# Kernel tuning notes

Hardware: AMD Instinct MI355X
Metric: run time of the kernel (lower is better)

The kernel has to match this reference:

```python
import jax, jax.numpy as jnp
import numpy as np

B, T, D, H = 2048, 1024, 64, 32  # batch, timesteps, input_size, hidden_dim


def setup_inputs() -> dict:
    key = jax.random.key(0)
    ks = jax.random.split(key, 11)
    k = 1.0 / np.sqrt(H)  # torch default GRU/Linear init range
    u = lambda kk, shape: jax.random.uniform(kk, shape, jnp.float32, -k, k)
    return {
        "x": jax.random.normal(ks[0], (B, T, D), jnp.float32),
        # layer 0 (input D -> hidden H); gate order r,z,n as in torch
        "w_ih0": u(ks[1], (3 * H, D)), "w_hh0": u(ks[2], (3 * H, H)),
        "b_ih0": u(ks[3], (3 * H,)),   "b_hh0": u(ks[4], (3 * H,)),
        # layer 1 (hidden H -> hidden H)
        "w_ih1": u(ks[5], (3 * H, H)), "w_hh1": u(ks[6], (3 * H, H)),
        "b_ih1": u(ks[7], (3 * H,)),   "b_hh1": u(ks[8], (3 * H,)),
        # classifier head H -> 1
        "w_cls": u(ks[9], (1, H)), "b_cls": u(ks[10], (1,)),
    }


def _gru_layer(x, w_ih, w_hh, b_ih, b_hh):
    # x: [B, T, Din]. Precompute the input contribution for all steps in one GEMM.
    gx = jnp.einsum('btd,gd->btg', x, w_ih) + b_ih  # [B, T, 3H]
    h0 = jnp.zeros((x.shape[0], H), x.dtype)

    def step(h, gx_t):
        gh = h @ w_hh.T + b_hh                       # [B, 3H]
        xr, xz, xn = jnp.split(gx_t, 3, axis=-1)
        hr, hz, hn = jnp.split(gh, 3, axis=-1)
        r = jax.nn.sigmoid(xr + hr)
        z = jax.nn.sigmoid(xz + hz)
        n = jnp.tanh(xn + r * hn)
        h_new = (1.0 - z) * n + z * h                # torch GRU update
        return h_new, h_new

    h_last, hs = jax.lax.scan(step, h0, jnp.swapaxes(gx, 0, 1))  # scan over T
    return jnp.swapaxes(hs, 0, 1), h_last            # [B, T, H], [B, H]


def reference(x, w_ih0, w_hh0, b_ih0, b_hh0, w_ih1, w_hh1, b_ih1, b_hh1, w_cls, b_cls):
    out0, h_last0 = _gru_layer(x, w_ih0, w_hh0, b_ih0, b_hh0)
    out1, h_last1 = _gru_layer(out0, w_ih1, w_hh1, b_ih1, b_hh1)
    y = jax.nn.sigmoid(h_last1 @ w_cls.T + b_cls)    # [B, 1]
    hidden = jnp.stack([h_last0, h_last1], axis=0)   # [2, B, H], like torch GRU hidden
    return y, hidden
```

## Files before the change

kernel.cpp:

```cpp
#include <hip/hip_runtime.h>
#include <hip/hip_bf16.h>

#define B_ 2048
#define T_ 1024

typedef short short8 __attribute__((ext_vector_type(8)));
typedef float floatx4 __attribute__((ext_vector_type(4)));

#define MFMA16(a, b, c) __builtin_amdgcn_mfma_f32_16x16x32_bf16((a), (b), (c), 0, 0, 0)
#define NLOG2E -1.4426950408889634f
#define TWOLOG2E 2.8853900817779268f

__device__ __forceinline__ unsigned short f2bf(float f) {
  union { float f; unsigned int i; } v;
  v.f = f;
  unsigned int r = v.i + 0x7fffu + ((v.i >> 16) & 1u);
  return (unsigned short)(r >> 16);
}

__device__ __forceinline__ unsigned int pack2(float lo, float hi) {
  __hip_bfloat162 h2;
  h2.x = __float2bfloat16(lo);
  h2.y = __float2bfloat16(hi);
  union { __hip_bfloat162 h; unsigned int u; } v;
  v.h = h2;
  return v.u;
}

__device__ __forceinline__ int rho32(int pb) {
  return 8 * ((pb >> 2) & 3) + 4 * (pb >> 4) + (pb & 3);
}

__device__ __forceinline__ short8 load_wfrag(const float* W, int K,
                                             int mt, int kt, int q, int c) {
  int p = 16 * mt + c;
  int blk = p >> 5;
  int pb = p & 31;
  int tr = 32 * blk + rho32(pb);
  float s = (blk < 2) ? NLOG2E : TWOLOG2E;
  const float* src = W + tr * K + 32 * kt + 8 * q;
  short8 out;
#pragma unroll
  for (int j = 0; j < 8; j++) out[j] = (short)f2bf(src[j] * s);
  return out;
}

__device__ __forceinline__ floatx4 bias_rz(const float* bih, const float* bhh,
                                           int tau, int q) {
  floatx4 f;
#pragma unroll
  for (int r = 0; r < 4; r++) {
    int p = 16 * tau + 4 * q + r;
    int idx = 32 * (p >> 5) + rho32(p & 31);
    f[r] = NLOG2E * (bih[idx] + bhh[idx]);
  }
  return f;
}
__device__ __forceinline__ floatx4 bias_n(const float* bias, int tau2, int q) {
  floatx4 f;
#pragma unroll
  for (int r = 0; r < 4; r++) {
    int pb = 16 * tau2 + 4 * q + r;
    f[r] = TWOLOG2E * bias[64 + rho32(pb)];
  }
  return f;
}

struct XRaw { float4 r0, r1, r2, r3; };
__device__ __forceinline__ XRaw xload(const float* p) {
  XRaw r;
  r.r0 = *(const float4*)p;
  r.r1 = *(const float4*)(p + 4);
  r.r2 = *(const float4*)(p + 32);
  r.r3 = *(const float4*)(p + 36);
  return r;
}
__device__ __forceinline__ void xconv(const XRaw& r, short8& f0, short8& f1) {
  union { short8 s8; unsigned int u[4]; } P;
  P.u[0] = pack2(r.r0.x, r.r0.y);
  P.u[1] = pack2(r.r0.z, r.r0.w);
  P.u[2] = pack2(r.r1.x, r.r1.y);
  P.u[3] = pack2(r.r1.z, r.r1.w);
  f0 = P.s8;
  P.u[0] = pack2(r.r2.x, r.r2.y);
  P.u[1] = pack2(r.r2.z, r.r2.w);
  P.u[2] = pack2(r.r3.x, r.r3.y);
  P.u[3] = pack2(r.r3.z, r.r3.w);
  f1 = P.s8;
}

__device__ __forceinline__ void gru_update(const floatx4* arz, const floatx4* anx,
                                           const floatx4* anh, float* h,
                                           short8* hf) {
#pragma unroll
  for (int t2 = 0; t2 < 2; t2++) {
#pragma unroll
    for (int r = 0; r < 4; r++) {
      float rr = __builtin_amdgcn_rcpf(1.0f + __builtin_amdgcn_exp2f(arz[t2][r]));
      float zz = __builtin_amdgcn_rcpf(1.0f + __builtin_amdgcn_exp2f(arz[2 + t2][r]));
      float u = fmaf(rr, anh[t2][r], anx[t2][r]);
      float nn = fmaf(-2.0f, __builtin_amdgcn_rcpf(1.0f + __builtin_amdgcn_exp2f(u)), 1.0f);
      int j = 4 * t2 + r;
      h[j] = fmaf(zz, h[j] - nn, nn);
    }
  }
  union { short8 s8; unsigned int u[4]; } P;
#pragma unroll
  for (int k2 = 0; k2 < 4; k2++) P.u[k2] = pack2(h[2 * k2], h[2 * k2 + 1]);
  *hf = P.s8;
}

#define LAYER0_MFMAS(xa, xb, h0in)                              \
  {                                                             \
    _Pragma("unroll") for (int tau = 0; tau < 4; tau++) {       \
      floatx4 a_ = MFMA16(Aih0[tau][0], (xa), brz0[tau]);       \
      a_ = MFMA16(Aih0[tau][1], (xb), a_);                      \
      arz0[tau] = MFMA16(Ahh0[tau], (h0in), a_);                \
    }                                                           \
    _Pragma("unroll") for (int t2 = 0; t2 < 2; t2++) {          \
      floatx4 a_ = MFMA16(Aih0[4 + t2][0], (xa), bnx0[t2]);     \
      anx0[t2] = MFMA16(Aih0[4 + t2][1], (xb), a_);             \
      anh0[t2] = MFMA16(Ahh0[4 + t2], (h0in), bnh0[t2]);        \
    }                                                           \
  }

#define LAYER1_MFMAS(h0in, h1in)                                \
  {                                                             \
    _Pragma("unroll") for (int tau = 0; tau < 4; tau++) {       \
      floatx4 a_ = MFMA16(Aih1[tau], (h0in), brz1[tau]);        \
      arz1[tau] = MFMA16(Ahh1[tau], (h1in), a_);                \
    }                                                           \
    _Pragma("unroll") for (int t2 = 0; t2 < 2; t2++) {          \
      anx1[t2] = MFMA16(Aih1[4 + t2], (h0in), bnx1[t2]);        \
      anh1[t2] = MFMA16(Ahh1[4 + t2], (h1in), bnh1[t2]);        \
    }                                                           \
  }

__global__ __launch_bounds__(64, 1) void gru_fused(
    const float* __restrict__ x,
    const float* __restrict__ wih0, const float* __restrict__ whh0,
    const float* __restrict__ bih0, const float* __restrict__ bhh0,
    const float* __restrict__ wih1, const float* __restrict__ whh1,
    const float* __restrict__ bih1, const float* __restrict__ bhh1,
    const float* __restrict__ wcls, const float* __restrict__ bcls,
    float* __restrict__ out) {
  const int lane = threadIdx.x & 63;
  const int q = lane >> 4;
  const int c = lane & 15;
  const int b = blockIdx.x * 16 + c;

  const float* px = x + ((size_t)b * T_) * 64 + 8 * q;
  XRaw q0 = xload(px);
  XRaw qA = xload(px + 64);
  XRaw qB = xload(px + 128);

  short8 Aih0[6][2], Ahh0[6], Aih1[6], Ahh1[6];
#pragma unroll
  for (int mt = 0; mt < 6; mt++) {
    Aih0[mt][0] = load_wfrag(wih0, 64, mt, 0, q, c);
    Aih0[mt][1] = load_wfrag(wih0, 64, mt, 1, q, c);
    Ahh0[mt] = load_wfrag(whh0, 32, mt, 0, q, c);
    Aih1[mt] = load_wfrag(wih1, 32, mt, 0, q, c);
    Ahh1[mt] = load_wfrag(whh1, 32, mt, 0, q, c);
  }
  floatx4 brz0[4], brz1[4], bnx0[2], bnh0[2], bnx1[2], bnh1[2];
#pragma unroll
  for (int tau = 0; tau < 4; tau++) {
    brz0[tau] = bias_rz(bih0, bhh0, tau, q);
    brz1[tau] = bias_rz(bih1, bhh1, tau, q);
  }
#pragma unroll
  for (int t2 = 0; t2 < 2; t2++) {
    bnx0[t2] = bias_n(bih0, t2, q);
    bnh0[t2] = bias_n(bhh0, t2, q);
    bnx1[t2] = bias_n(bih1, t2, q);
    bnh1[t2] = bias_n(bhh1, t2, q);
  }

  float h0[8], h1[8];
  short8 h0f_p, h0f_n, h1f;
#pragma unroll
  for (int j = 0; j < 8; j++) {
    h0[j] = 0.f;
    h1[j] = 0.f;
    h0f_p[j] = 0;
    h0f_n[j] = 0;
    h1f[j] = 0;
  }

  floatx4 arz0[4], anx0[2], anh0[2];
  floatx4 arz1[4], anx1[2], anh1[2];
  short8 xfA0, xfA1, xfB0, xfB1;

  {
    short8 x00, x01;
    xconv(q0, x00, x01);
    LAYER0_MFMAS(x00, x01, h0f_p);
    gru_update(arz0, anx0, anh0, h0, &h0f_p);
    xconv(qA, xfA0, xfA1);
  }

  int i = 1;
  for (; i + 1 < T_; i += 2) {
    qA = xload(px + (size_t)(i + 2) * 64);
    LAYER0_MFMAS(xfA0, xfA1, h0f_p);
    LAYER1_MFMAS(h0f_p, h1f);
    gru_update(arz0, anx0, anh0, h0, &h0f_n);
    gru_update(arz1, anx1, anh1, h1, &h1f);
    xconv(qB, xfB0, xfB1);

    {
      const int t3 = (i + 3 < T_) ? (i + 3) : (T_ - 1);
      qB = xload(px + (size_t)t3 * 64);
    }
    LAYER0_MFMAS(xfB0, xfB1, h0f_n);
    LAYER1_MFMAS(h0f_n, h1f);
    gru_update(arz0, anx0, anh0, h0, &h0f_p);
    gru_update(arz1, anx1, anh1, h1, &h1f);
    xconv(qA, xfA0, xfA1);
  }

  LAYER0_MFMAS(xfA0, xfA1, h0f_p);
  LAYER1_MFMAS(h0f_p, h1f);
  gru_update(arz0, anx0, anh0, h0, &h0f_n);
  gru_update(arz1, anx1, anh1, h1, &h1f);

  LAYER1_MFMAS(h0f_n, h1f);
  gru_update(arz1, anx1, anh1, h1, &h1f);

  float* oh0 = out + 2048 + (size_t)b * 32 + 8 * q;
  float* oh1 = oh0 + 65536;
  *(float4*)oh0 = make_float4(h0[0], h0[1], h0[2], h0[3]);
  *(float4*)(oh0 + 4) = make_float4(h0[4], h0[5], h0[6], h0[7]);
  *(float4*)oh1 = make_float4(h1[0], h1[1], h1[2], h1[3]);
  *(float4*)(oh1 + 4) = make_float4(h1[4], h1[5], h1[6], h1[7]);

  float wc[8];
#pragma unroll
  for (int j = 0; j < 8; j++) wc[j] = wcls[8 * q + j];
  float acc = 0.f;
#pragma unroll
  for (int j = 0; j < 8; j++) acc = fmaf(h1[j], wc[j], acc);
  acc += __shfl_xor(acc, 16, 64);
  acc += __shfl_xor(acc, 32, 64);
  if (q == 0) {
    float pre = acc + bcls[0];
    out[b] = __builtin_amdgcn_rcpf(1.0f + __builtin_amdgcn_exp2f(NLOG2E * pre));
  }
}

extern "C" void kernel_launch(void* const* d_in, const int* in_sizes, int n_in,
                              void* d_out, int out_size, void* d_ws, size_t ws_size,
                              hipStream_t stream) {
  const float* x    = (const float*)d_in[0];
  const float* wih0 = (const float*)d_in[1];
  const float* whh0 = (const float*)d_in[2];
  const float* bih0 = (const float*)d_in[3];
  const float* bhh0 = (const float*)d_in[4];
  const float* wih1 = (const float*)d_in[5];
  const float* whh1 = (const float*)d_in[6];
  const float* bih1 = (const float*)d_in[7];
  const float* bhh1 = (const float*)d_in[8];
  const float* wcls = (const float*)d_in[9];
  const float* bcls = (const float*)d_in[10];
  float* out = (float*)d_out;

  gru_fused<<<dim3(B_ / 16), dim3(64), 0, stream>>>(
      x, wih0, whh0, bih0, bhh0, wih1, whh1, bih1, bhh1, wcls, bcls, out);
}
```

Before: 1.693 ms.

## Split the two GRU layers across two pipelined wavefronts using LDS handoff

The block grows from one wavefront to two. Wave 0 runs layer 0 and publishes each bf16 hidden state to a double-buffered LDS slot. Wave 1 consumes that state and runs layer 1 one step behind, with the two waves kept in lockstep by s_barrier. This roughly halves the serial per-step dependency chain per wave and spreads the weight fragments across two waves' registers. In exchange it adds a workgroup barrier and an LDS round-trip on every timestep. The layer-1 MFMA order is also changed so the recurrent h1 products issue first, ahead of the h0 read from LDS.

Result: no change. 1.687 ms (-0.3%).

```diff
diff --git a/kernel.cpp b/kernel.cpp
--- a/kernel.cpp
+++ b/kernel.cpp
@@ -115,28 +115,33 @@
     _Pragma("unroll") for (int tau = 0; tau < 4; tau++) {       \
       floatx4 a_ = MFMA16(Aih0[tau][0], (xa), brz0[tau]);       \
       a_ = MFMA16(Aih0[tau][1], (xb), a_);                      \
-      arz0[tau] = MFMA16(Ahh0[tau], (h0in), a_);                \
+      arz[tau] = MFMA16(Ahh0[tau], (h0in), a_);                 \
     }                                                           \
     _Pragma("unroll") for (int t2 = 0; t2 < 2; t2++) {          \
       floatx4 a_ = MFMA16(Aih0[4 + t2][0], (xa), bnx0[t2]);     \
-      anx0[t2] = MFMA16(Aih0[4 + t2][1], (xb), a_);             \
-      anh0[t2] = MFMA16(Ahh0[4 + t2], (h0in), bnh0[t2]);        \
+      anx[t2] = MFMA16(Aih0[4 + t2][1], (xb), a_);              \
+      anh[t2] = MFMA16(Ahh0[4 + t2], (h0in), bnh0[t2]);         \
     }                                                           \
   }
 
 #define LAYER1_MFMAS(h0in, h1in)                                \
   {                                                             \
-    _Pragma("unroll") for (int tau = 0; tau < 4; tau++) {       \
-      floatx4 a_ = MFMA16(Aih1[tau], (h0in), brz1[tau]);        \
-      arz1[tau] = MFMA16(Ahh1[tau], (h1in), a_);                \
-    }                                                           \
-    _Pragma("unroll") for (int t2 = 0; t2 < 2; t2++) {          \
-      anx1[t2] = MFMA16(Aih1[4 + t2], (h0in), bnx1[t2]);        \
-      anh1[t2] = MFMA16(Ahh1[4 + t2], (h1in), bnh1[t2]);        \
-    }                                                           \
-  }
-
-__global__ __launch_bounds__(64, 1) void gru_fused(
+    floatx4 t_[4];                                              \
+    _Pragma("unroll") for (int tau = 0; tau < 4; tau++)         \
+      t_[tau] = MFMA16(Ahh1[tau], (h1in), brz1[tau]);           \
+    _Pragma("unroll") for (int t2 = 0; t2 < 2; t2++)            \
+      anh[t2] = MFMA16(Ahh1[4 + t2], (h1in), bnh1[t2]);         \
+    _Pragma("unroll") for (int tau = 0; tau < 4; tau++)         \
+      arz[tau] = MFMA16(Aih1[tau], (h0in), t_[tau]);            \
+    _Pragma("unroll") for (int t2 = 0; t2 < 2; t2++)            \
+      anx[t2] = MFMA16(Aih1[4 + t2], (h0in), bnx1[t2]);         \
+  }
+
+#define LGKM0_BARRIER()                                   \
+  asm volatile("s_waitcnt lgkmcnt(0)" ::: "memory");      \
+  __builtin_amdgcn_s_barrier()
+
+__global__ __launch_bounds__(128, 1) void gru_fused(
     const float* __restrict__ x,
     const float* __restrict__ wih0, const float* __restrict__ whh0,
     const float* __restrict__ bih0, const float* __restrict__ bhh0,
@@ -145,107 +150,148 @@
     const float* __restrict__ wcls, const float* __restrict__ bcls,
     float* __restrict__ out) {
   const int lane = threadIdx.x & 63;
+  const int w = threadIdx.x >> 6;
   const int q = lane >> 4;
   const int c = lane & 15;
   const int b = blockIdx.x * 16 + c;
 
-  const float* px = x + ((size_t)b * T_) * 64 + 8 * q;
-  XRaw q0 = xload(px);
-  XRaw qA = xload(px + 64);
-  XRaw qB = xload(px + 128);
-
-  short8 Aih0[6][2], Ahh0[6], Aih1[6], Ahh1[6];
-#pragma unroll
-  for (int mt = 0; mt < 6; mt++) {
-    Aih0[mt][0] = load_wfrag(wih0, 64, mt, 0, q, c);
-    Aih0[mt][1] = load_wfrag(wih0, 64, mt, 1, q, c);
-    Ahh0[mt] = load_wfrag(whh0, 32, mt, 0, q, c);
-    Aih1[mt] = load_wfrag(wih1, 32, mt, 0, q, c);
-    Ahh1[mt] = load_wfrag(whh1, 32, mt, 0, q, c);
-  }
-  floatx4 brz0[4], brz1[4], bnx0[2], bnh0[2], bnx1[2], bnh1[2];
-#pragma unroll
-  for (int tau = 0; tau < 4; tau++) {
-    brz0[tau] = bias_rz(bih0, bhh0, tau, q);
-    brz1[tau] = bias_rz(bih1, bhh1, tau, q);
-  }
-#pragma unroll
-  for (int t2 = 0; t2 < 2; t2++) {
-    bnx0[t2] = bias_n(bih0, t2, q);
-    bnh0[t2] = bias_n(bhh0, t2, q);
-    bnx1[t2] = bias_n(bih1, t2, q);
-    bnh1[t2] = bias_n(bhh1, t2, q);
-  }
-
-  float h0[8], h1[8];
-  short8 h0f_p, h0f_n, h1f;
-#pragma unroll
-  for (int j = 0; j < 8; j++) {
-    h0[j] = 0.f;
-    h1[j] = 0.f;
-    h0f_p[j] = 0;
-    h0f_n[j] = 0;
-    h1f[j] = 0;
-  }
-
-  floatx4 arz0[4], anx0[2], anh0[2];
-  floatx4 arz1[4], anx1[2], anh1[2];
-  short8 xfA0, xfA1, xfB0, xfB1;
-
-  {
-    short8 x00, x01;
-    xconv(q0, x00, x01);
-    LAYER0_MFMAS(x00, x01, h0f_p);
-    gru_update(arz0, anx0, anh0, h0, &h0f_p);
-    xconv(qA, xfA0, xfA1);
-  }
-
-  int i = 1;
-  for (; i + 1 < T_; i += 2) {
-    qA = xload(px + (size_t)(i + 2) * 64);
-    LAYER0_MFMAS(xfA0, xfA1, h0f_p);
-    LAYER1_MFMAS(h0f_p, h1f);
-    gru_update(arz0, anx0, anh0, h0, &h0f_n);
-    gru_update(arz1, anx1, anh1, h1, &h1f);
-    xconv(qB, xfB0, xfB1);
+  __shared__ short8 hslot[2][64];
+
+  floatx4 arz[4], anx[2], anh[2];
+
+  if (w == 0) {
+    const float* px = x + ((size_t)b * T_) * 64 + 8 * q;
+    XRaw q0 = xload(px);
+    XRaw qA = xload(px + 64);
+    XRaw qB = xload(px + 128);
+
+    short8 Aih0[6][2], Ahh0[6];
+#pragma unroll
+    for (int mt = 0; mt < 6; mt++) {
+      Aih0[mt][0] = load_wfrag(wih0, 64, mt, 0, q, c);
+      Aih0[mt][1] = load_wfrag(wih0, 64, mt, 1, q, c);
+      Ahh0[mt] = load_wfrag(whh0, 32, mt, 0, q, c);
+    }
+    floatx4 brz0[4], bnx0[2], bnh0[2];
+#pragma unroll
+    for (int tau = 0; tau < 4; tau++) brz0[tau] = bias_rz(bih0, bhh0, tau, q);
+#pragma unroll
+    for (int t2 = 0; t2 < 2; t2++) {
+      bnx0[t2] = bias_n(bih0, t2, q);
+      bnh0[t2] = bias_n(bhh0, t2, q);
+    }
+
+    float h0[8];
+    short8 h0f;
+#pragma unroll
+    for (int j = 0; j < 8; j++) { h0[j] = 0.f; h0f[j] = 0; }
+
+    short8 xfA0, xfA1, xfB0, xfB1;
 
     {
-      const int t3 = (i + 3 < T_) ? (i + 3) : (T_ - 1);
-      qB = xload(px + (size_t)t3 * 64);
-    }
-    LAYER0_MFMAS(xfB0, xfB1, h0f_n);
-    LAYER1_MFMAS(h0f_n, h1f);
-    gru_update(arz0, anx0, anh0, h0, &h0f_p);
-    gru_update(arz1, anx1, anh1, h1, &h1f);
-    xconv(qA, xfA0, xfA1);
-  }
-
-  LAYER0_MFMAS(xfA0, xfA1, h0f_p);
-  LAYER1_MFMAS(h0f_p, h1f);
-  gru_update(arz0, anx0, anh0, h0, &h0f_n);
-  gru_update(arz1, anx1, anh1, h1, &h1f);
-
-  LAYER1_MFMAS(h0f_n, h1f);
-  gru_update(arz1, anx1, anh1, h1, &h1f);
-
-  float* oh0 = out + 2048 + (size_t)b * 32 + 8 * q;
-  float* oh1 = oh0 + 65536;
-  *(float4*)oh0 = make_float4(h0[0], h0[1], h0[2], h0[3]);
-  *(float4*)(oh0 + 4) = make_float4(h0[4], h0[5], h0[6], h0[7]);
-  *(float4*)oh1 = make_float4(h1[0], h1[1], h1[2], h1[3]);
-  *(float4*)(oh1 + 4) = make_float4(h1[4], h1[5], h1[6], h1[7]);
-
-  float wc[8];
-#pragma unroll
-  for (int j = 0; j < 8; j++) wc[j] = wcls[8 * q + j];
-  float acc = 0.f;
-#pragma unroll
-  for (int j = 0; j < 8; j++) acc = fmaf(h1[j], wc[j], acc);
-  acc += __shfl_xor(acc, 16, 64);
-  acc += __shfl_xor(acc, 32, 64);
-  if (q == 0) {
-    float pre = acc + bcls[0];
-    out[b] = __builtin_amdgcn_rcpf(1.0f + __builtin_amdgcn_exp2f(NLOG2E * pre));
+      short8 x00, x01;
+      xconv(q0, x00, x01);
+      LAYER0_MFMAS(x00, x01, h0f);
+      gru_update(arz, anx, anh, h0, &h0f);
+      hslot[0][lane] = h0f;
+      LGKM0_BARRIER();
+      xconv(qA, xfA0, xfA1);
+    }
+
+    for (int i = 1; i + 1 < T_; i += 2) {
+      qA = xload(px + (size_t)(i + 2) * 64);
+      LAYER0_MFMAS(xfA0, xfA1, h0f);
+      gru_update(arz, anx, anh, h0, &h0f);
+      hslot[1][lane] = h0f;
+      LGKM0_BARRIER();
+      xconv(qB, xfB0, xfB1);
+
+      {
+        const int t3 = (i + 3 < T_) ? (i + 3) : (T_ - 1);
+        qB = xload(px + (size_t)t3 * 64);
+      }
+      LAYER0_MFMAS(xfB0, xfB1, h0f);
+      gru_update(arz, anx, anh, h0, &h0f);
+      hslot[0][lane] = h0f;
+      LGKM0_BARRIER();
+      xconv(qA, xfA0, xfA1);
+    }
+
+    LAYER0_MFMAS(xfA0, xfA1, h0f);
+    gru_update(arz, anx, anh, h0, &h0f);
+    hslot[1][lane] = h0f;
+    LGKM0_BARRIER();
+
+    float* oh0 = out + 2048 + (size_t)b * 32 + 8 * q;
+    *(float4*)oh0 = make_float4(h0[0], h0[1], h0[2], h0[3]);
+    *(float4*)(oh0 + 4) = make_float4(h0[4], h0[5], h0[6], h0[7]);
+  } else {
+    short8 Aih1[6], Ahh1[6];
+#pragma unroll
+    for (int mt = 0; mt < 6; mt++) {
+      Aih1[mt] = load_wfrag(wih1, 32, mt, 0, q, c);
+      Ahh1[mt] = load_wfrag(whh1, 32, mt, 0, q, c);
+    }
+    floatx4 brz1[4], bnx1[2], bnh1[2];
+#pragma unroll
+    for (int tau = 0; tau < 4; tau++) brz1[tau] = bias_rz(bih1, bhh1, tau, q);
+#pragma unroll
+    for (int t2 = 0; t2 < 2; t2++) {
+      bnx1[t2] = bias_n(bih1, t2, q);
+      bnh1[t2] = bias_n(bhh1, t2, q);
+    }
+    float wc[8];
+#pragma unroll
+    for (int j = 0; j < 8; j++) wc[j] = wcls[8 * q + j];
+
+    float h1[8];
+    short8 h1f;
+#pragma unroll
+    for (int j = 0; j < 8; j++) { h1[j] = 0.f; h1f[j] = 0; }
+
+    __builtin_amdgcn_s_barrier();
+
+    for (int j = 0; j < T_ - 3; j += 2) {
+      asm volatile("" ::: "memory");
+      short8 h0in = hslot[0][lane];
+      LAYER1_MFMAS(h0in, h1f);
+      gru_update(arz, anx, anh, h1, &h1f);
+      __builtin_amdgcn_s_barrier();
+
+      asm volatile("" ::: "memory");
+      short8 h0in2 = hslot[1][lane];
+      LAYER1_MFMAS(h0in2, h1f);
+      gru_update(arz, anx, anh, h1, &h1f);
+      __builtin_amdgcn_s_barrier();
+    }
+
+    {
+      asm volatile("" ::: "memory");
+      short8 h0in = hslot[0][lane];
+      LAYER1_MFMAS(h0in, h1f);
+      gru_update(arz, anx, anh, h1, &h1f);
+      __builtin_amdgcn_s_barrier();
+    }
+    {
+      asm volatile("" ::: "memory");
+      short8 h0in = hslot[1][lane];
+      LAYER1_MFMAS(h0in, h1f);
+      gru_update(arz, anx, anh, h1, &h1f);
+    }
+
+    float* oh1 = out + 2048 + 65536 + (size_t)b * 32 + 8 * q;
+    *(float4*)oh1 = make_float4(h1[0], h1[1], h1[2], h1[3]);
+    *(float4*)(oh1 + 4) = make_float4(h1[4], h1[5], h1[6], h1[7]);
+
+    float acc = 0.f;
+#pragma unroll
+    for (int j = 0; j < 8; j++) acc = fmaf(h1[j], wc[j], acc);
+    acc += __shfl_xor(acc, 16, 64);
+    acc += __shfl_xor(acc, 32, 64);
+    if (q == 0) {
+      float pre = acc + bcls[0];
+      out[b] = __builtin_amdgcn_rcpf(1.0f + __builtin_amdgcn_exp2f(NLOG2E * pre));
+    }
   }
 }
 
@@ -265,6 +311,6 @@
   const float* bcls = (const float*)d_in[10];
   float* out = (float*)d_out;
 
-  gru_fused<<<dim3(B_ / 16), dim3(64), 0, stream>>>(
+  gru_fused<<<dim3(B_ / 16), dim3(128), 0, stream>>>(
       x, wih0, whh0, bih0, bhh0, wih1, whh1, bih1, bhh1, wcls, bcls, out);
 }
```
